# Kernel optimization log

Hardware: AMD Instinct MI355X
Metric: run time of the kernel (lower is better)

## Reference

```python
import jax, jax.numpy as jnp
import numpy as np

B, N, M, K = 8, 9225, 4096, 32
D = 2          # coordinate dim
HID = 64       # MLP hidden
DOUT = 16      # MLP output / f_y channels


def setup_inputs() -> dict:
    key = jax.random.key(0)
    ks = jax.random.split(key, 10)
    y = jax.random.uniform(ks[0], (B, N, D), dtype=jnp.float32)
    x = jax.random.uniform(ks[1], (B, M, D), dtype=jnp.float32)
    f_y = jax.random.uniform(ks[2], (B, N, DOUT), dtype=jnp.float32)
    weights = jax.random.uniform(ks[3], (B, N), dtype=jnp.float32)
    neighbors_index = jax.random.randint(ks[4], (B, M, K), 0, N, dtype=jnp.int64)
    drop = jax.random.uniform(ks[5], (B, M, K)) < 0.1
    neighbors_index = jnp.where(drop, jnp.int64(-1), neighbors_index)
    # LinearChannelMLP params: 4 -> 64 -> 16, gelu between
    W1 = jax.random.normal(ks[6], (2 * D, HID), dtype=jnp.float32) * (1.0 / np.sqrt(2 * D))
    b1 = jnp.zeros((HID,), dtype=jnp.float32)
    W2 = jax.random.normal(ks[7], (HID, DOUT), dtype=jnp.float32) * (1.0 / np.sqrt(HID))
    b2 = jnp.zeros((DOUT,), dtype=jnp.float32)
    return {"y": y, "x": x, "f_y": f_y, "weights": weights,
            "W1": W1, "b1": b1, "W2": W2, "b2": b2,
            "neighbors_index": neighbors_index}


def _batched_gather(table, idx):
    # table: [B, N, ...], idx: [B, M, K] -> [B, M, K, ...]
    return jax.vmap(lambda t, i: t[i])(table, idx)


def reference(y, x, f_y, weights, W1, b1, W2, b2, neighbors_index):
    idx = jnp.where(neighbors_index == -1, 0, neighbors_index)      # [B,M,K]
    valid = (neighbors_index != -1).astype(y.dtype)[..., None]      # [B,M,K,1]

    rep_y = _batched_gather(y, idx)                                 # [B,M,K,D]
    in_f = _batched_gather(f_y, idx)                                # [B,M,K,DOUT]
    self_x = jnp.broadcast_to(x[:, :, None, :], rep_y.shape)        # [B,M,K,D]

    agg = jnp.concatenate([rep_y, self_x], axis=-1)                 # [B,M,K,2D]
    h = jax.nn.gelu(agg @ W1 + b1, approximate=False)               # [B,M,K,HID]
    kval = h @ W2 + b2                                              # [B,M,K,DOUT]

    kval = kval * in_f                                              # linear transform: k(x,y)*f(y)
    w_nbr = _batched_gather(weights, idx)[..., None]                # [B,M,K,1]
    kval = kval * w_nbr * valid
    return kval.sum(axis=2)                                         # [B,M,DOUT]
```

## Files before the change

### kernel.cpp

```cpp
#include <hip/hip_runtime.h>
#include <hip/hip_bf16.h>
#include <math.h>

#define B_    8
#define N_    9225
#define M_    4096
#define K_    32
#define HID_  64
#define DOUT_ 16

typedef __attribute__((ext_vector_type(8))) short short8;
typedef __attribute__((ext_vector_type(4))) float floatx4;
typedef __attribute__((ext_vector_type(2))) float f32x2;
typedef __attribute__((ext_vector_type(4))) unsigned uint4v;

static __device__ __forceinline__ short f2bf(float f) {
    __hip_bfloat16 h = __float2bfloat16(f);
    return __builtin_bit_cast(short, h);
}
static __device__ __forceinline__ f32x2 splat2(float v) { return (f32x2){v, v}; }

static __device__ __forceinline__ unsigned cvtpk(float a, float b) {
    unsigned r;
    asm("v_cvt_pk_bf16_f32 %0, %1, %2" : "=v"(r) : "v"(a), "v"(b));
    return r;
}
static __device__ __forceinline__ float pk_lo_f(unsigned u) {
    return __builtin_bit_cast(float, u << 16);
}
static __device__ __forceinline__ float pk_hi_f(unsigned u) {
    return __builtin_bit_cast(float, u & 0xffff0000u);
}

static __device__ __forceinline__ void gload_lds16(const float* g, float* lds_base) {
    __builtin_amdgcn_global_load_lds(
        (const __attribute__((address_space(1))) void*)g,
        (__attribute__((address_space(3))) void*)lds_base, 16, 0, 0);
}

static __device__ __forceinline__ float row16_sum(float v) {
    int t;
    t = __builtin_amdgcn_update_dpp(0, __builtin_bit_cast(int, v), 0x111, 0xF, 0xF, true);
    v += __builtin_bit_cast(float, t);
    t = __builtin_amdgcn_update_dpp(0, __builtin_bit_cast(int, v), 0x112, 0xF, 0xF, true);
    v += __builtin_bit_cast(float, t);
    t = __builtin_amdgcn_update_dpp(0, __builtin_bit_cast(int, v), 0x114, 0xF, 0xF, true);
    v += __builtin_bit_cast(float, t);
    t = __builtin_amdgcn_update_dpp(0, __builtin_bit_cast(int, v), 0x118, 0xF, 0xF, true);
    v += __builtin_bit_cast(float, t);
    return v;
}

__global__ __launch_bounds__(256, 4) void it_kernel(
    const float* __restrict__ y,
    const float* __restrict__ x,
    const float* __restrict__ f_y,
    const float* __restrict__ weights,
    const float* __restrict__ W1,
    const float* __restrict__ b1,
    const float* __restrict__ W2,
    const float* __restrict__ b2,
    const int*   __restrict__ nbr,
    float*       __restrict__ out)
{
    __shared__ unsigned short lut[2048];
    __shared__ float stg[4][8][256];

    const int tid  = threadIdx.x;
    #pragma unroll
    for (int i = tid; i < 2048; i += 256) {
        const float xi = (float)(i - 1024) * 0.0078125f;
        const float g  = 0.5f * xi * (1.0f + erff(xi * 0.70710678f));
        lut[i] = (unsigned short)f2bf(g);
    }

    const int lane = tid & 63;
    const int q    = lane >> 4;
    const int nlo  = lane & 15;
    const bool q0  = (q == 0);

    const int blk   = blockIdx.x;
    const int batch = blk & 7;
    const int pblk  = blk >> 3;
    const int wid   = tid >> 6;
    const int row0  = __builtin_amdgcn_readfirstlane(batch * M_ + pblk * 16 + wid * 4);
    const int bbase = batch * N_;

    int raw[8];
    #pragma unroll
    for (int ph = 0; ph < 8; ++ph) {
        const int it = ph >> 1, h = ph & 1;
        raw[ph] = nbr[(size_t)(row0 + it) * K_ + h * 16 + nlo];
    }

    short8 w1h[4];
    #pragma unroll
    for (int t = 0; t < 4; ++t) {
        #pragma unroll
        for (int jj = 0; jj < 4; ++jj) {
            const float wv = W1[jj * HID_ + t * 16 + nlo] * 128.0f;
            const short b  = q0 ? f2bf(wv) : (short)0;
            w1h[t][jj]     = b;
            w1h[t][jj + 4] = b;
        }
    }

    short8 w2f[2];
    #pragma unroll
    for (int ch = 0; ch < 2; ++ch)
        #pragma unroll
        for (int jj = 0; jj < 8; ++jj) {
            const int H = (ch * 2 + (jj >> 2)) * 16 + q * 4 + (jj & 3);
            w2f[ch][jj] = f2bf(W2[H * DOUT_ + nlo]);
        }

    floatx4 biasC[4];
    #pragma unroll
    for (int t = 0; t < 4; ++t) {
        const floatx4 b1q = *(const floatx4*)(b1 + t * 16 + q * 4);
        biasC[t] = b1q * 128.0f + 1024.5f;
    }
    const floatx4 b2r = *(const floatx4*)(b2 + q * 4);

    unsigned xw_h[4], xw_l[4];
    #pragma unroll
    for (int it = 0; it < 4; ++it) {
        const float2 xv = *(const float2*)(x + (size_t)(row0 + it) * 2);
        const unsigned hw = cvtpk(xv.x, xv.y);
        xw_h[it] = hw;
        xw_l[it] = cvtpk(xv.x - pk_lo_f(hw), xv.y - pk_hi_f(hw));
    }

    float2 yv2[8]; float sw[8];
    #pragma unroll
    for (int i = 0; i < 8; ++i) yv2[i] = (float2){0.0f, 0.0f};
    #pragma unroll
    for (int P = 0; P < 8; ++P) {
        const int rv  = raw[P];
        const int vld = rv >= 0;
        const int bn  = bbase + (vld ? rv : 0);
        gload_lds16(f_y + (size_t)bn * 16 + q * 4, &stg[wid][P][0]);
        const float wv_ = weights[bn];
        sw[P] = vld ? wv_ : 0.0f;
        if (q0) yv2[P] = *(const float2*)(y + (size_t)bn * 2);
    }

    __syncthreads();
    __builtin_amdgcn_sched_barrier(0);

    float partial[4] = {0.f, 0.f, 0.f, 0.f};
    #pragma unroll
    for (int ph = 0; ph < 8; ++ph) {
        const int it = ph >> 1;

        const floatx4 fvp = *(const floatx4*)&stg[wid][ph][lane * 4];

        const float y0 = yv2[ph].x, y1 = yv2[ph].y;
        const unsigned yw_h = cvtpk(y0, y1);
        const unsigned yw_l = cvtpk(y0 - pk_lo_f(yw_h), y1 - pk_hi_f(yw_h));
        const uint4v bw = { yw_h, xw_h[it], yw_l, xw_l[it] };
        const short8 bfull = __builtin_bit_cast(short8, bw);

        floatx4 a1[4];
        #pragma unroll
        for (int t = 0; t < 4; ++t)
            a1[t] = __builtin_amdgcn_mfma_f32_16x16x32_bf16(w1h[t], bfull, biasC[t], 0, 0, 0);

        unsigned hw[8];
        #pragma unroll
        for (int t = 0; t < 4; ++t) {
            f32x2 i01 = {a1[t][0], a1[t][1]};
            f32x2 i23 = {a1[t][2], a1[t][3]};
            i01 = __builtin_elementwise_min(
                      __builtin_elementwise_max(i01, splat2(0.0f)), splat2(2047.0f));
            i23 = __builtin_elementwise_min(
                      __builtin_elementwise_max(i23, splat2(0.0f)), splat2(2047.0f));
            const unsigned short l0 = lut[(unsigned)i01[0]];
            const unsigned short l1 = lut[(unsigned)i01[1]];
            const unsigned short l2 = lut[(unsigned)i23[0]];
            const unsigned short l3 = lut[(unsigned)i23[1]];
            hw[t * 2 + 0] = (unsigned)l0 | ((unsigned)l1 << 16);
            hw[t * 2 + 1] = (unsigned)l2 | ((unsigned)l3 << 16);
        }
        const uint4v h0w = { hw[0], hw[1], hw[2], hw[3] };
        const uint4v h1w = { hw[4], hw[5], hw[6], hw[7] };
        const short8 hf0 = __builtin_bit_cast(short8, h0w);
        const short8 hf1 = __builtin_bit_cast(short8, h1w);

        floatx4 acc = b2r;
        acc = __builtin_amdgcn_mfma_f32_16x16x32_bf16(w2f[0], hf0, acc, 0, 0, 0);
        acc = __builtin_amdgcn_mfma_f32_16x16x32_bf16(w2f[1], hf1, acc, 0, 0, 0);

        const float s = sw[ph];
        #pragma unroll
        for (int r = 0; r < 4; ++r)
            partial[r] = fmaf(acc[r], fvp[r] * s, partial[r]);

        if (ph & 1) {
            #pragma unroll
            for (int r = 0; r < 4; ++r) partial[r] = row16_sum(partial[r]);
            if (nlo == 15) {
                floatx4 o = {partial[0], partial[1], partial[2], partial[3]};
                *(floatx4*)(out + (size_t)(row0 + it) * DOUT_ + q * 4) = o;
            }
            #pragma unroll
            for (int r = 0; r < 4; ++r) partial[r] = 0.f;
        }
    }
}

extern "C" void kernel_launch(void* const* d_in, const int* in_sizes, int n_in,
                              void* d_out, int out_size, void* d_ws, size_t ws_size,
                              hipStream_t stream) {
    const float* y   = (const float*)d_in[0];
    const float* x   = (const float*)d_in[1];
    const float* f_y = (const float*)d_in[2];
    const float* w   = (const float*)d_in[3];
    const float* W1  = (const float*)d_in[4];
    const float* b1  = (const float*)d_in[5];
    const float* W2  = (const float*)d_in[6];
    const float* b2  = (const float*)d_in[7];
    const int*   nbr = (const int*)d_in[8];
    float* out = (float*)d_out;

    dim3 grid(B_ * M_ / 16), block(256);
    hipLaunchKernelGGL(it_kernel, grid, block, 0, stream,
                       y, x, f_y, w, W1, b1, W2, b2, nbr, out);
}
```

Before: 102.9 us.

## Switch MLP matmuls to 32x32x16 MFMA tiles processing two rows per pass

Restructures the per-wave MLP evaluation to use 32x32x16 bf16 MFMA instead of 16x16x32, so each pass covers 32 neighbor columns (two query rows interleaved) and halves the number of loop iterations. Weight, bias and f_y staging layouts are remapped to the 32x32 accumulator layout, with the second-layer product split into two independent accumulator chains. The intent is to cut MFMA instruction count, the wasted zero-padded K, and loop overhead. In exchange it raises register pressure (16-wide accumulators), so launch bounds drop from 4 to 3 blocks per CU.

```diff
diff --git a/kernel.cpp b/kernel.cpp
--- a/kernel.cpp
+++ b/kernel.cpp
@@ -13,6 +13,7 @@
 typedef __attribute__((ext_vector_type(4))) float floatx4;
 typedef __attribute__((ext_vector_type(2))) float f32x2;
 typedef __attribute__((ext_vector_type(4))) unsigned uint4v;
+typedef __attribute__((ext_vector_type(16))) float f32x16;
 
 static __device__ __forceinline__ short f2bf(float f) {
     __hip_bfloat16 h = __float2bfloat16(f);
@@ -51,7 +52,7 @@
     return v;
 }
 
-__global__ __launch_bounds__(256, 4) void it_kernel(
+__global__ __launch_bounds__(256, 3) void it_kernel(
     const float* __restrict__ y,
     const float* __restrict__ x,
     const float* __restrict__ f_y,
@@ -64,7 +65,7 @@
     float*       __restrict__ out)
 {
     __shared__ unsigned short lut[2048];
-    __shared__ float stg[4][8][256];
+    __shared__ float stg[4][4][2][256];
 
     const int tid  = threadIdx.x;
     #pragma unroll
@@ -75,9 +76,10 @@
     }
 
     const int lane = tid & 63;
-    const int q    = lane >> 4;
+    const int col  = lane & 31;
+    const int hi   = lane >> 5;
     const int nlo  = lane & 15;
-    const bool q0  = (q == 0);
+    const int rsel = (lane >> 4) & 1;
 
     const int blk   = blockIdx.x;
     const int batch = blk & 7;
@@ -86,125 +88,143 @@
     const int row0  = __builtin_amdgcn_readfirstlane(batch * M_ + pblk * 16 + wid * 4);
     const int bbase = batch * N_;
 
-    int raw[8];
-    #pragma unroll
-    for (int ph = 0; ph < 8; ++ph) {
-        const int it = ph >> 1, h = ph & 1;
-        raw[ph] = nbr[(size_t)(row0 + it) * K_ + h * 16 + nlo];
-    }
-
-    short8 w1h[4];
-    #pragma unroll
-    for (int t = 0; t < 4; ++t) {
-        #pragma unroll
-        for (int jj = 0; jj < 4; ++jj) {
-            const float wv = W1[jj * HID_ + t * 16 + nlo] * 128.0f;
-            const short b  = q0 ? f2bf(wv) : (short)0;
-            w1h[t][jj]     = b;
-            w1h[t][jj + 4] = b;
-        }
-    }
-
-    short8 w2f[2];
-    #pragma unroll
-    for (int ch = 0; ch < 2; ++ch)
+    int raw[4];
+    #pragma unroll
+    for (int p = 0; p < 4; ++p) {
+        const int roff = 2 * (p >> 1) + rsel;
+        const int kidx = (p & 1) * 16 + nlo;
+        raw[p] = nbr[(size_t)(row0 + roff) * K_ + kidx];
+    }
+
+    short8 w1a[2];
+    #pragma unroll
+    for (int t = 0; t < 2; ++t)
         #pragma unroll
         for (int jj = 0; jj < 8; ++jj) {
-            const int H = (ch * 2 + (jj >> 2)) * 16 + q * 4 + (jj & 3);
-            w2f[ch][jj] = f2bf(W2[H * DOUT_ + nlo]);
-        }
-
-    floatx4 biasC[4];
-    #pragma unroll
-    for (int t = 0; t < 4; ++t) {
-        const floatx4 b1q = *(const floatx4*)(b1 + t * 16 + q * 4);
-        biasC[t] = b1q * 128.0f + 1024.5f;
-    }
-    const floatx4 b2r = *(const floatx4*)(b2 + q * 4);
+            const float wv = W1[(jj & 3) * HID_ + t * 32 + col] * 128.0f;
+            w1a[t][jj] = (hi == 0) ? f2bf(wv) : (short)0;
+        }
+
+    short8 w2a[4];
+    #pragma unroll
+    for (int m = 0; m < 4; ++m)
+        #pragma unroll
+        for (int jj = 0; jj < 8; ++jj) {
+            const int H = (jj & 3) + 8 * ((2 * m + (jj >> 2)) & 3) + 4 * hi + 32 * (m >> 1);
+            w2a[m][jj] = (col < 16) ? f2bf(W2[H * DOUT_ + col]) : (short)0;
+        }
+
+    f32x16 biasC[2];
+    #pragma unroll
+    for (int t = 0; t < 2; ++t)
+        #pragma unroll
+        for (int reg = 0; reg < 16; ++reg)
+            biasC[t][reg] = b1[t * 32 + (reg & 3) + 8 * (reg >> 2) + 4 * hi] * 128.0f + 1024.5f;
+
+    f32x16 b2C;
+    #pragma unroll
+    for (int reg = 0; reg < 16; ++reg)
+        b2C[reg] = (reg < 8) ? b2[(reg & 3) + 8 * (reg >> 2) + 4 * hi] : 0.0f;
+    f32x16 zero16;
+    #pragma unroll
+    for (int reg = 0; reg < 16; ++reg) zero16[reg] = 0.0f;
 
     unsigned xw_h[4], xw_l[4];
     #pragma unroll
     for (int it = 0; it < 4; ++it) {
         const float2 xv = *(const float2*)(x + (size_t)(row0 + it) * 2);
-        const unsigned hw = cvtpk(xv.x, xv.y);
-        xw_h[it] = hw;
-        xw_l[it] = cvtpk(xv.x - pk_lo_f(hw), xv.y - pk_hi_f(hw));
-    }
-
-    float2 yv2[8]; float sw[8];
-    #pragma unroll
-    for (int i = 0; i < 8; ++i) yv2[i] = (float2){0.0f, 0.0f};
-    #pragma unroll
-    for (int P = 0; P < 8; ++P) {
-        const int rv  = raw[P];
-        const int vld = rv >= 0;
-        const int bn  = bbase + (vld ? rv : 0);
-        gload_lds16(f_y + (size_t)bn * 16 + q * 4, &stg[wid][P][0]);
+        const unsigned hw_ = cvtpk(xv.x, xv.y);
+        xw_h[it] = hw_;
+        xw_l[it] = cvtpk(xv.x - pk_lo_f(hw_), xv.y - pk_hi_f(hw_));
+    }
+
+    float2 yv[4]; float sw[4];
+    #pragma unroll
+    for (int i = 0; i < 4; ++i) yv[i] = (float2){0.0f, 0.0f};
+    #pragma unroll
+    for (int p = 0; p < 4; ++p) {
+        const int rv = raw[p];
+        const int bn = bbase + (rv >= 0 ? rv : 0);
+        gload_lds16(f_y + (size_t)bn * 16 + 4 * hi,     &stg[wid][p][0][0]);
+        gload_lds16(f_y + (size_t)bn * 16 + 4 * hi + 8, &stg[wid][p][1][0]);
         const float wv_ = weights[bn];
-        sw[P] = vld ? wv_ : 0.0f;
-        if (q0) yv2[P] = *(const float2*)(y + (size_t)bn * 2);
-    }
-
+        sw[p] = (rv >= 0) ? wv_ : 0.0f;
+        if (lane < 32) yv[p] = *(const float2*)(y + (size_t)bn * 2);
+    }
     __syncthreads();
     __builtin_amdgcn_sched_barrier(0);
 
-    float partial[4] = {0.f, 0.f, 0.f, 0.f};
-    #pragma unroll
-    for (int ph = 0; ph < 8; ++ph) {
-        const int it = ph >> 1;
-
-        const floatx4 fvp = *(const floatx4*)&stg[wid][ph][lane * 4];
-
-        const float y0 = yv2[ph].x, y1 = yv2[ph].y;
-        const unsigned yw_h = cvtpk(y0, y1);
-        const unsigned yw_l = cvtpk(y0 - pk_lo_f(yw_h), y1 - pk_hi_f(yw_h));
-        const uint4v bw = { yw_h, xw_h[it], yw_l, xw_l[it] };
-        const short8 bfull = __builtin_bit_cast(short8, bw);
-
-        floatx4 a1[4];
-        #pragma unroll
-        for (int t = 0; t < 4; ++t)
-            a1[t] = __builtin_amdgcn_mfma_f32_16x16x32_bf16(w1h[t], bfull, biasC[t], 0, 0, 0);
-
-        unsigned hw[8];
-        #pragma unroll
-        for (int t = 0; t < 4; ++t) {
-            f32x2 i01 = {a1[t][0], a1[t][1]};
-            f32x2 i23 = {a1[t][2], a1[t][3]};
-            i01 = __builtin_elementwise_min(
-                      __builtin_elementwise_max(i01, splat2(0.0f)), splat2(2047.0f));
-            i23 = __builtin_elementwise_min(
-                      __builtin_elementwise_max(i23, splat2(0.0f)), splat2(2047.0f));
-            const unsigned short l0 = lut[(unsigned)i01[0]];
-            const unsigned short l1 = lut[(unsigned)i01[1]];
-            const unsigned short l2 = lut[(unsigned)i23[0]];
-            const unsigned short l3 = lut[(unsigned)i23[1]];
-            hw[t * 2 + 0] = (unsigned)l0 | ((unsigned)l1 << 16);
-            hw[t * 2 + 1] = (unsigned)l2 | ((unsigned)l3 << 16);
-        }
-        const uint4v h0w = { hw[0], hw[1], hw[2], hw[3] };
-        const uint4v h1w = { hw[4], hw[5], hw[6], hw[7] };
-        const short8 hf0 = __builtin_bit_cast(short8, h0w);
-        const short8 hf1 = __builtin_bit_cast(short8, h1w);
-
-        floatx4 acc = b2r;
-        acc = __builtin_amdgcn_mfma_f32_16x16x32_bf16(w2f[0], hf0, acc, 0, 0, 0);
-        acc = __builtin_amdgcn_mfma_f32_16x16x32_bf16(w2f[1], hf1, acc, 0, 0, 0);
-
-        const float s = sw[ph];
-        #pragma unroll
-        for (int r = 0; r < 4; ++r)
-            partial[r] = fmaf(acc[r], fvp[r] * s, partial[r]);
-
-        if (ph & 1) {
+    unsigned ywh[4], ywl[4];
+    #pragma unroll
+    for (int p = 0; p < 4; ++p) {
+        const float y0 = yv[p].x, y1 = yv[p].y;
+        const unsigned hw_ = cvtpk(y0, y1);
+        ywh[p] = hw_;
+        ywl[p] = cvtpk(y0 - pk_lo_f(hw_), y1 - pk_hi_f(hw_));
+    }
+
+    float partial[8] = {0.f, 0.f, 0.f, 0.f, 0.f, 0.f, 0.f, 0.f};
+    #pragma unroll
+    for (int p = 0; p < 4; ++p) {
+        const int rA = 2 * (p >> 1);
+
+        const unsigned xh_ = rsel ? xw_h[rA + 1] : xw_h[rA];
+        const unsigned xl_ = rsel ? xw_l[rA + 1] : xw_l[rA];
+        const uint4v bwv = { ywh[p], xh_, ywl[p], xl_ };
+        const short8 bf = __builtin_bit_cast(short8, bwv);
+
+        const f32x16 a1lo = __builtin_amdgcn_mfma_f32_32x32x16_bf16(w1a[0], bf, biasC[0], 0, 0, 0);
+        const f32x16 a1hi = __builtin_amdgcn_mfma_f32_32x32x16_bf16(w1a[1], bf, biasC[1], 0, 0, 0);
+
+        const floatx4 fv0 = *(const floatx4*)&stg[wid][p][0][lane * 4];
+        const floatx4 fv1 = *(const floatx4*)&stg[wid][p][1][lane * 4];
+        const float s = sw[p];
+        const floatx4 g0 = fv0 * s, g1 = fv1 * s;
+
+        short8 bm[4];
+        #pragma unroll
+        for (int m = 0; m < 4; ++m) {
+            unsigned words[4];
             #pragma unroll
-            for (int r = 0; r < 4; ++r) partial[r] = row16_sum(partial[r]);
+            for (int w = 0; w < 4; ++w) {
+                const int t    = m >> 1;
+                const int u    = (2 * m + (w >> 1)) & 3;
+                const int regA = (u << 2) | ((2 * w) & 3);
+                const float iA = t ? a1hi[regA]     : a1lo[regA];
+                const float iB = t ? a1hi[regA + 1] : a1lo[regA + 1];
+                f32x2 iv = {iA, iB};
+                iv = __builtin_elementwise_min(
+                         __builtin_elementwise_max(iv, splat2(0.0f)), splat2(2047.0f));
+                const unsigned short lA = lut[(unsigned)iv[0]];
+                const unsigned short lB = lut[(unsigned)iv[1]];
+                words[w] = (unsigned)lA | ((unsigned)lB << 16);
+            }
+            bm[m] = __builtin_bit_cast(short8, (uint4v){words[0], words[1], words[2], words[3]});
+        }
+
+        f32x16 acc01 = __builtin_amdgcn_mfma_f32_32x32x16_bf16(w2a[0], bm[0], b2C, 0, 0, 0);
+        f32x16 acc23 = __builtin_amdgcn_mfma_f32_32x32x16_bf16(w2a[2], bm[2], zero16, 0, 0, 0);
+        acc01 = __builtin_amdgcn_mfma_f32_32x32x16_bf16(w2a[1], bm[1], acc01, 0, 0, 0);
+        acc23 = __builtin_amdgcn_mfma_f32_32x32x16_bf16(w2a[3], bm[3], acc23, 0, 0, 0);
+
+        #pragma unroll
+        for (int r = 0; r < 4; ++r) {
+            partial[r]     = fmaf(acc01[r]     + acc23[r],     g0[r], partial[r]);
+            partial[4 + r] = fmaf(acc01[4 + r] + acc23[4 + r], g1[r], partial[4 + r]);
+        }
+
+        if (p & 1) {
+            #pragma unroll
+            for (int r = 0; r < 8; ++r) partial[r] = row16_sum(partial[r]);
             if (nlo == 15) {
-                floatx4 o = {partial[0], partial[1], partial[2], partial[3]};
-                *(floatx4*)(out + (size_t)(row0 + it) * DOUT_ + q * 4) = o;
+                const int row = row0 + rA + rsel;
+                floatx4 o0 = {partial[0], partial[1], partial[2], partial[3]};
+                floatx4 o1 = {partial[4], partial[5], partial[6], partial[7]};
+                *(floatx4*)(out + (size_t)row * DOUT_ + 4 * hi)     = o0;
+                *(floatx4*)(out + (size_t)row * DOUT_ + 4 * hi + 8) = o1;
             }
             #pragma unroll
-            for (int r = 0; r < 4; ++r) partial[r] = 0.f;
+            for (int r = 0; r < 8; ++r) partial[r] = 0.f;
         }
     }
 }
```

After: 114.5 us. +11.3%, slower.
